# Kernel optimization log

Measured on AMD Instinct MI355X. Metric: run time of the kernel, lower is better.

## Reference

```python
import jax, jax.numpy as jnp
import numpy as np

B, S, D = 1, 2048, 2048
H, KVH, HD = 16, 4, 128  # n_heads, n_kv_heads, head_dim; n_rep = H // KVH
NEG = -1e9


def setup_inputs() -> dict:
    key = jax.random.key(0)
    ks = jax.random.split(key, 5)
    x = jax.random.normal(ks[0], (B, S, D), dtype=jnp.float32)
    sd = 1.0 / np.sqrt(D)
    wq = jax.random.normal(ks[1], (D, H * HD), dtype=jnp.float32) * sd
    wk = jax.random.normal(ks[2], (D, KVH * HD), dtype=jnp.float32) * sd
    wv = jax.random.normal(ks[3], (D, KVH * HD), dtype=jnp.float32) * sd
    wo = jax.random.normal(ks[4], (H * HD, D), dtype=jnp.float32) * sd
    # RoPE frequencies: theta = 10000, pairs of dims
    inv_freq = 1.0 / (10000.0 ** (jnp.arange(0, HD, 2, dtype=jnp.float32) / HD))  # [HD/2]
    t = jnp.arange(S, dtype=jnp.float32)
    freqs = jnp.outer(t, inv_freq)  # [S, HD/2]
    freqs_cos = jnp.cos(freqs)
    freqs_sin = jnp.sin(freqs)
    # additive causal mask [S, S]
    mask = jnp.where(jnp.tril(jnp.ones((S, S), dtype=bool)), 0.0, NEG).astype(jnp.float32)
    return {"x": x, "wq": wq, "wk": wk, "wv": wv, "wo": wo,
            "freqs_cos": freqs_cos, "freqs_sin": freqs_sin, "mask": mask}


def _rope(t, cos, sin):
    # t: [B, S, h, HD]; cos/sin: [S, HD/2] -> broadcast [1, S, 1, HD/2]
    tr = t.reshape(*t.shape[:-1], HD // 2, 2)
    t0, t1 = tr[..., 0], tr[..., 1]
    c = cos[None, :, None, :]
    s = sin[None, :, None, :]
    o0 = t0 * c - t1 * s
    o1 = t0 * s + t1 * c
    return jnp.stack([o0, o1], axis=-1).reshape(t.shape)


def reference(x, wq, wk, wv, wo, freqs_cos, freqs_sin, mask):
    n_rep = H // KVH
    xq = (x @ wq).reshape(B, S, H, HD)
    xk = (x @ wk).reshape(B, S, KVH, HD)
    xv = (x @ wv).reshape(B, S, KVH, HD)
    xq = _rope(xq, freqs_cos, freqs_sin)
    xk = _rope(xk, freqs_cos, freqs_sin)
    # repeat KV heads for GQA -> [B, S, H, HD]
    xk = jnp.repeat(xk, n_rep, axis=2)
    xv = jnp.repeat(xv, n_rep, axis=2)
    # [B, H, S, HD]
    q = xq.transpose(0, 2, 1, 3)
    k = xk.transpose(0, 2, 1, 3)
    v = xv.transpose(0, 2, 1, 3)
    scores = jnp.einsum('bhqd,bhkd->bhqk', q, k) / jnp.sqrt(jnp.float32(HD))
    scores = scores + mask[None, None, :, :]
    probs = jax.nn.softmax(scores.astype(jnp.float32), axis=-1).astype(q.dtype)
    out = jnp.einsum('bhqk,bhkd->bhqd', probs, v)
    out = out.transpose(0, 2, 1, 3).reshape(B, S, H * HD)
    return out @ wo
```

## Files before the change

### kernel.cpp

```cpp
#include <hip/hip_runtime.h>
#include <stdint.h>

#define S_LEN 2048
#define DMODEL 2048
#define NH 16
#define NKV 4
#define HD 128

typedef __attribute__((ext_vector_type(8))) short bf16x8_t;
typedef __attribute__((ext_vector_type(4))) short bf16x4_t;
typedef __attribute__((ext_vector_type(4))) float f32x4;

static __device__ __forceinline__ short f2bf(float f) {
  uint32_t x = __float_as_uint(f);
  uint32_t r = (x + 0x7FFFu + ((x >> 16) & 1u)) >> 16;
  return (short)r;
}

static __device__ __forceinline__ void gload16(const void* g, void* l) {
  __builtin_amdgcn_global_load_lds((const __attribute__((address_space(1))) void*)g,
                                   (__attribute__((address_space(3))) void*)l, 16, 0, 0);
}

__global__ void cvt_bf16(const float* __restrict__ in, short* __restrict__ out, int n8) {
  int idx = blockIdx.x * 256 + threadIdx.x;
  if (idx >= n8) return;
  const float4* p = (const float4*)in + 2 * (size_t)idx;
  float4 a = p[0], b = p[1];
  bf16x8_t o;
  o[0] = f2bf(a.x); o[1] = f2bf(a.y); o[2] = f2bf(a.z); o[3] = f2bf(a.w);
  o[4] = f2bf(b.x); o[5] = f2bf(b.y); o[6] = f2bf(b.z); o[7] = f2bf(b.w);
  ((bf16x8_t*)out)[idx] = o;
}

__global__ void transpose_f32_bf16(const float* __restrict__ in, short* __restrict__ out,
                                   int inStride, int outStride,
                                   long zInOff, long zOutOff) {
  __shared__ float tile[32][33];
  in  += (size_t)blockIdx.z * zInOff;
  out += (size_t)blockIdx.z * zOutOff;
  int c0 = blockIdx.x * 32, r0 = blockIdx.y * 32;
  int tx = threadIdx.x, ty = threadIdx.y;
  for (int i = ty; i < 32; i += 8)
    tile[i][tx] = in[(size_t)(r0 + i) * inStride + c0 + tx];
  __syncthreads();
  for (int i = ty; i < 32; i += 8)
    out[(size_t)(c0 + i) * outStride + r0 + tx] = f2bf(tile[tx][i]);
}

__global__ void rope_heads(const float* __restrict__ xf, const float* __restrict__ fc,
                           const float* __restrict__ fs, short* __restrict__ outp,
                           int rowStride) {
  int s = blockIdx.x;
  int i = threadIdx.x;
  int h = blockIdx.y * blockDim.y + threadIdx.y;
  float c = fc[s * 64 + i], sn = fs[s * 64 + i];
  const float* xr = xf + (size_t)s * rowStride + h * HD;
  float t0 = xr[2 * i], t1 = xr[2 * i + 1];
  float o0 = t0 * c - t1 * sn;
  float o1 = t0 * sn + t1 * c;
  short* orow = outp + ((size_t)h * S_LEN + s) * HD;
  uint32_t pk = (uint32_t)(uint16_t)f2bf(o0) | ((uint32_t)(uint16_t)f2bf(o1) << 16);
  *(uint32_t*)&orow[2 * i] = pk;
}

__global__ __launch_bounds__(128) void gemm_bt(const short* __restrict__ A,
                                               const short* __restrict__ Bt,
                                               float* __restrict__ C,
                                               int M, int N, int K) {
  __shared__ char smem[12288];
  const int tid = threadIdx.x;
  const int wid = tid >> 6, lane = tid & 63;
  const int lq = lane & 15, g = lane >> 4;
  const int bm = blockIdx.y * 128, bn = blockIdx.x * 64;

  f32x4 acc[4][4] = {};

  const short* Asrc[4];
  const short* Bsrc[2];
#pragma unroll
  for (int u = 0; u < 4; u++) {
    int p = wid * 64 + u * 128 + lane;
    Asrc[u] = A + (size_t)(bm + (p >> 2)) * K + (p & 3) * 8;
  }
#pragma unroll
  for (int u = 0; u < 2; u++) {
    int p = wid * 64 + u * 128 + lane;
    Bsrc[u] = Bt + (size_t)(bn + (p >> 2)) * K + (p & 3) * 8;
  }
  char* la = smem;
  char* lb = smem + 8192;

  for (int k0 = 0; k0 < K; k0 += 32) {
    __syncthreads();
#pragma unroll
    for (int u = 0; u < 4; u++)
      gload16(Asrc[u] + k0, la + wid * 1024 + u * 2048);
#pragma unroll
    for (int u = 0; u < 2; u++)
      gload16(Bsrc[u] + k0, lb + wid * 1024 + u * 2048);
    __syncthreads();
    bf16x8_t af[4], bfr[4];
#pragma unroll
    for (int mi = 0; mi < 4; mi++)
      af[mi] = *(const bf16x8_t*)(la + (wid * 64 + mi * 16 + lq) * 64 + g * 16);
#pragma unroll
    for (int ni = 0; ni < 4; ni++)
      bfr[ni] = *(const bf16x8_t*)(lb + (ni * 16 + lq) * 64 + g * 16);
#pragma unroll
    for (int mi = 0; mi < 4; mi++)
#pragma unroll
      for (int ni = 0; ni < 4; ni++)
        acc[mi][ni] = __builtin_amdgcn_mfma_f32_16x16x32_bf16(af[mi], bfr[ni], acc[mi][ni], 0, 0, 0);
  }
#pragma unroll
  for (int mi = 0; mi < 4; mi++) {
#pragma unroll
    for (int r = 0; r < 4; r++) {
      int row = bm + wid * 64 + mi * 16 + g * 4 + r;
      float* Crow = C + (size_t)row * N + bn;
#pragma unroll
      for (int ni = 0; ni < 4; ni++)
        Crow[ni * 16 + lq] = acc[mi][ni][r];
    }
  }
}

__global__ __launch_bounds__(128) void flash_attn(const short* __restrict__ Q,
                                                  const short* __restrict__ Kb,
                                                  const short* __restrict__ Vt,
                                                  short* __restrict__ Oatt) {
  __shared__ char smem[65536];
  const int h = blockIdx.y, kvh = h >> 2;
  const int pair = blockIdx.x;
  const int wid = threadIdx.x >> 6, lane = threadIdx.x & 63;
  const int lq = lane & 15, g = lane >> 4;
  const float scale2 = 0.0883883476483184f * 1.4426950408889634f;
  const short* Kh = Kb + (size_t)kvh * S_LEN * HD;
  const short* Vh = Vt + (size_t)kvh * HD * S_LEN;

  int kOff[8], vOff[8];
#pragma unroll
  for (int u = 0; u < 8; u++) {
    int p = wid * 64 + u * 128 + lane;
    int kr = p >> 4, kc = (p & 15) ^ (kr & 7);
    kOff[u] = kr * HD + kc * 8;
    int vd = p >> 3, vc = (p & 7) ^ (vd & 7);
    vOff[u] = vd * S_LEN + vc * 8;
  }
  const int swz = lq & 7;

  for (int pass = 0; pass < 2; pass++) {
    const int qi = pass ? (63 - pair) : pair;
    const int q0 = qi * 32 + wid * 16;
    const int ntiles = (qi >> 1) + 1;
    const int q_abs = q0 + lq;

    const short* Qb = Q + ((size_t)h * S_LEN + q0) * HD;
    bf16x8_t qf[4];
#pragma unroll
    for (int kk = 0; kk < 4; kk++)
      qf[kk] = *(const bf16x8_t*)(Qb + lq * HD + kk * 32 + g * 8);

    f32x4 oa[8] = {};
    float m_run = -1e30f, l_run = 0.f;

#pragma unroll
    for (int u = 0; u < 8; u++) {
      gload16(Kh + kOff[u], smem + wid * 1024 + u * 2048);
      gload16(Vh + vOff[u], smem + 16384 + wid * 1024 + u * 2048);
    }
    __syncthreads();

    for (int t = 0; t < ntiles; t++) {
      const int cur = t & 1;
      const int kv0 = t * 64;
      if (t + 1 < ntiles) {
        const short* Ks = Kh + (size_t)(kv0 + 64) * HD;
        const short* Vs = Vh + kv0 + 64;
        char* dk = smem + (cur ^ 1) * 32768;
        char* dv = dk + 16384;
#pragma unroll
        for (int u = 0; u < 8; u++) {
          gload16(Ks + kOff[u], dk + wid * 1024 + u * 2048);
          gload16(Vs + vOff[u], dv + wid * 1024 + u * 2048);
        }
      }
      const char* lk = smem + cur * 32768;
      const char* lv = lk + 16384;

      f32x4 sc[4] = {};
#pragma unroll
      for (int sub = 0; sub < 4; sub++) {
        const char* krow = lk + (sub * 16 + lq) * 256;
#pragma unroll
        for (int kk = 0; kk < 4; kk++) {
          bf16x8_t kf = *(const bf16x8_t*)(krow + (((kk * 4 + g) ^ swz) << 4));
          sc[sub] = __builtin_amdgcn_mfma_f32_16x16x32_bf16(kf, qf[kk], sc[sub], 0, 0, 0);
        }
      }
      float s16[16];
      if (t == ntiles - 1) {
#pragma unroll
        for (int sub = 0; sub < 4; sub++)
#pragma unroll
          for (int r = 0; r < 4; r++) {
            int kva = kv0 + sub * 16 + 4 * g + r;
            s16[sub * 4 + r] = (kva <= q_abs) ? sc[sub][r] * scale2 : -1e30f;
          }
      } else {
#pragma unroll
        for (int sub = 0; sub < 4; sub++)
#pragma unroll
          for (int r = 0; r < 4; r++)
            s16[sub * 4 + r] = sc[sub][r] * scale2;
      }
      float mx = s16[0];
#pragma unroll
      for (int j = 1; j < 16; j++) mx = fmaxf(mx, s16[j]);
      mx = fmaxf(mx, __shfl_xor(mx, 16));
      mx = fmaxf(mx, __shfl_xor(mx, 32));
      float m_new = fmaxf(m_run, mx);
      float p16[16], psum = 0.f;
#pragma unroll
      for (int j = 0; j < 16; j++) { p16[j] = exp2f(s16[j] - m_new); psum += p16[j]; }
      psum += __shfl_xor(psum, 16);
      psum += __shfl_xor(psum, 32);
      float f = exp2f(m_run - m_new);
      l_run = l_run * f + psum;
      m_run = m_new;

      bf16x8_t pf0, pf1;
#pragma unroll
      for (int j = 0; j < 8; j++) { pf0[j] = f2bf(p16[j]); pf1[j] = f2bf(p16[8 + j]); }
      float fr[4];
#pragma unroll
      for (int r = 0; r < 4; r++) fr[r] = __shfl(f, 4 * g + r);
#pragma unroll
      for (int nt = 0; nt < 8; nt++)
#pragma unroll
        for (int r = 0; r < 4; r++) oa[nt][r] *= fr[r];

      const int gh = g >> 1;
#pragma unroll
      for (int nt = 0; nt < 8; nt++) {
        const char* vrow = lv + (nt * 16 + lq) * 128 + (g & 1) * 8;
#pragma unroll
        for (int ks = 0; ks < 2; ks++) {
          bf16x4_t v0 = *(const bf16x4_t*)(vrow + (((ks * 4 + gh) ^ swz) << 4));
          bf16x4_t v1 = *(const bf16x4_t*)(vrow + (((ks * 4 + 2 + gh) ^ swz) << 4));
          bf16x8_t vf;
#pragma unroll
          for (int j = 0; j < 4; j++) { vf[j] = v0[j]; vf[4 + j] = v1[j]; }
          oa[nt] = __builtin_amdgcn_mfma_f32_16x16x32_bf16(ks ? pf1 : pf0, vf, oa[nt], 0, 0, 0);
        }
      }
      __syncthreads();
    }

    float lr[4];
#pragma unroll
    for (int r = 0; r < 4; r++) lr[r] = 1.0f / __shfl(l_run, 4 * g + r);
#pragma unroll
    for (int nt = 0; nt < 8; nt++)
#pragma unroll
      for (int r = 0; r < 4; r++) {
        int row = q0 + 4 * g + r;
        Oatt[(size_t)row * (NH * HD) + h * HD + nt * 16 + lq] = f2bf(oa[nt][r] * lr[r]);
      }
  }
}

extern "C" void kernel_launch(void* const* d_in, const int* in_sizes, int n_in,
                              void* d_out, int out_size, void* d_ws, size_t ws_size,
                              hipStream_t stream) {
  const float* x  = (const float*)d_in[0];
  const float* wq = (const float*)d_in[1];
  const float* wk = (const float*)d_in[2];
  const float* wv = (const float*)d_in[3];
  const float* wo = (const float*)d_in[4];
  const float* fc = (const float*)d_in[5];
  const float* fs = (const float*)d_in[6];
  float* out = (float*)d_out;

  char* ws = (char*)d_ws;
  const size_t MB = 1024 * 1024;
  if (ws_size < 72 * MB) return;
  short* xb    = (short*)(ws);
  short* wqkvT = (short*)(ws + 8 * MB);
  short* woT   = (short*)(ws + 20 * MB);
  float* xqkvf = (float*)(ws + 28 * MB);
  short* qbf   = (short*)(ws + 52 * MB);
  short* kbf   = (short*)(ws + 60 * MB);
  short* vT    = (short*)(ws + 62 * MB);
  short* abf   = (short*)(ws + 64 * MB);

  dim3 tb(32, 8);
  cvt_bf16<<<2048, 256, 0, stream>>>(x, xb, (S_LEN * DMODEL) / 8);
  transpose_f32_bf16<<<dim3(64, 64, 1), tb, 0, stream>>>(wq, wqkvT, 2048, 2048, 0, 0);
  transpose_f32_bf16<<<dim3(16, 64, 1), tb, 0, stream>>>(wk, wqkvT + (size_t)2048 * 2048, 512, 2048, 0, 0);
  transpose_f32_bf16<<<dim3(16, 64, 1), tb, 0, stream>>>(wv, wqkvT + (size_t)2560 * 2048, 512, 2048, 0, 0);
  transpose_f32_bf16<<<dim3(64, 64, 1), tb, 0, stream>>>(wo, woT, 2048, 2048, 0, 0);

  gemm_bt<<<dim3(48, 16), 128, 0, stream>>>(xb, wqkvT, xqkvf, 2048, 3072, 2048);

  rope_heads<<<dim3(2048, 4), dim3(64, 4), 0, stream>>>(xqkvf, fc, fs, qbf, 3072);
  rope_heads<<<dim3(2048, 1), dim3(64, 4), 0, stream>>>(xqkvf + 2048, fc, fs, kbf, 3072);
  transpose_f32_bf16<<<dim3(4, 64, 4), tb, 0, stream>>>(xqkvf + 2560, vT, 3072, 2048, 128, 128L * 2048);

  flash_attn<<<dim3(32, 16), 128, 0, stream>>>(qbf, kbf, vT, abf);

  gemm_bt<<<dim3(32, 16), 128, 0, stream>>>(abf, woT, out, 2048, 2048, 2048);
}
```

Baseline: 330.5 us.

## Emit bf16 QKV from GEMM, fold softmax scale into Q, restructure flash attention

The QKV GEMM now writes bf16 instead of fp32, so the rope and V-transpose kernels read half the bytes. The softmax scale is folded into Q during rope. Flash attention moves from 128-thread blocks that each process two paired 32-row query tiles with double-buffered K/V to 256-thread blocks handling one 64-row tile with a single buffer and 32KB of shared memory. It also adds a lazy rescale that skips the output correction when the running max rises by less than a threshold, plus s_setprio around the MFMA sections. The trade-off is an extra bf16 rounding of the QKV projections, loss of load/compute overlap, and causal imbalance because the pairing is dropped.

```diff
diff --git a/kernel.cpp b/kernel.cpp
--- a/kernel.cpp
+++ b/kernel.cpp
@@ -48,25 +48,43 @@
     out[(size_t)(c0 + i) * outStride + r0 + tx] = f2bf(tile[tx][i]);
 }
 
-__global__ void rope_heads(const float* __restrict__ xf, const float* __restrict__ fc,
+__global__ void transpose_bf16(const short* __restrict__ in, short* __restrict__ out,
+                               int inStride, int outStride,
+                               long zInOff, long zOutOff) {
+  __shared__ short tile[32][33];
+  in  += (size_t)blockIdx.z * zInOff;
+  out += (size_t)blockIdx.z * zOutOff;
+  int c0 = blockIdx.x * 32, r0 = blockIdx.y * 32;
+  int tx = threadIdx.x, ty = threadIdx.y;
+  for (int i = ty; i < 32; i += 8)
+    tile[i][tx] = in[(size_t)(r0 + i) * inStride + c0 + tx];
+  __syncthreads();
+  for (int i = ty; i < 32; i += 8)
+    out[(size_t)(c0 + i) * outStride + r0 + tx] = tile[tx][i];
+}
+
+__global__ void rope_heads(const short* __restrict__ xf, const float* __restrict__ fc,
                            const float* __restrict__ fs, short* __restrict__ outp,
-                           int rowStride) {
+                           int rowStride, float oscale) {
   int s = blockIdx.x;
   int i = threadIdx.x;
   int h = blockIdx.y * blockDim.y + threadIdx.y;
   float c = fc[s * 64 + i], sn = fs[s * 64 + i];
-  const float* xr = xf + (size_t)s * rowStride + h * HD;
-  float t0 = xr[2 * i], t1 = xr[2 * i + 1];
-  float o0 = t0 * c - t1 * sn;
-  float o1 = t0 * sn + t1 * c;
+  const short* xr = xf + (size_t)s * rowStride + h * HD;
+  uint32_t w = *(const uint32_t*)&xr[2 * i];
+  float t0 = __uint_as_float((w & 0xFFFFu) << 16);
+  float t1 = __uint_as_float(w & 0xFFFF0000u);
+  float o0 = (t0 * c - t1 * sn) * oscale;
+  float o1 = (t0 * sn + t1 * c) * oscale;
   short* orow = outp + ((size_t)h * S_LEN + s) * HD;
   uint32_t pk = (uint32_t)(uint16_t)f2bf(o0) | ((uint32_t)(uint16_t)f2bf(o1) << 16);
   *(uint32_t*)&orow[2 * i] = pk;
 }
 
+template <bool BF16OUT>
 __global__ __launch_bounds__(128) void gemm_bt(const short* __restrict__ A,
                                                const short* __restrict__ Bt,
-                                               float* __restrict__ C,
+                                               void* __restrict__ Cv,
                                                int M, int N, int K) {
   __shared__ char smem[12288];
   const int tid = threadIdx.x;
@@ -118,31 +136,38 @@
 #pragma unroll
     for (int r = 0; r < 4; r++) {
       int row = bm + wid * 64 + mi * 16 + g * 4 + r;
-      float* Crow = C + (size_t)row * N + bn;
-#pragma unroll
-      for (int ni = 0; ni < 4; ni++)
-        Crow[ni * 16 + lq] = acc[mi][ni][r];
-    }
-  }
-}
-
-__global__ __launch_bounds__(128) void flash_attn(const short* __restrict__ Q,
-                                                  const short* __restrict__ Kb,
-                                                  const short* __restrict__ Vt,
-                                                  short* __restrict__ Oatt) {
-  __shared__ char smem[65536];
+      if (BF16OUT) {
+        short* Crow = (short*)Cv + (size_t)row * N + bn;
+#pragma unroll
+        for (int ni = 0; ni < 4; ni++)
+          Crow[ni * 16 + lq] = f2bf(acc[mi][ni][r]);
+      } else {
+        float* Crow = (float*)Cv + (size_t)row * N + bn;
+#pragma unroll
+        for (int ni = 0; ni < 4; ni++)
+          Crow[ni * 16 + lq] = acc[mi][ni][r];
+      }
+    }
+  }
+}
+
+__global__ __launch_bounds__(256, 3) void flash_attn(const short* __restrict__ Q,
+                                                     const short* __restrict__ Kb,
+                                                     const short* __restrict__ Vt,
+                                                     short* __restrict__ Oatt) {
+  __shared__ char smem[32768];
   const int h = blockIdx.y, kvh = h >> 2;
-  const int pair = blockIdx.x;
-  const int wid = threadIdx.x >> 6, lane = threadIdx.x & 63;
+  const int qi = 31 - blockIdx.x;
+  const int tid = threadIdx.x;
+  const int wid = tid >> 6, lane = tid & 63;
   const int lq = lane & 15, g = lane >> 4;
-  const float scale2 = 0.0883883476483184f * 1.4426950408889634f;
   const short* Kh = Kb + (size_t)kvh * S_LEN * HD;
   const short* Vh = Vt + (size_t)kvh * HD * S_LEN;
 
-  int kOff[8], vOff[8];
-#pragma unroll
-  for (int u = 0; u < 8; u++) {
-    int p = wid * 64 + u * 128 + lane;
+  int kOff[4], vOff[4];
+#pragma unroll
+  for (int u = 0; u < 4; u++) {
+    int p = u * 256 + tid;
     int kr = p >> 4, kc = (p & 15) ^ (kr & 7);
     kOff[u] = kr * HD + kc * 8;
     int vd = p >> 3, vc = (p & 7) ^ (vd & 7);
@@ -150,125 +175,118 @@
   }
   const int swz = lq & 7;
 
-  for (int pass = 0; pass < 2; pass++) {
-    const int qi = pass ? (63 - pair) : pair;
-    const int q0 = qi * 32 + wid * 16;
-    const int ntiles = (qi >> 1) + 1;
-    const int q_abs = q0 + lq;
-
-    const short* Qb = Q + ((size_t)h * S_LEN + q0) * HD;
-    bf16x8_t qf[4];
-#pragma unroll
-    for (int kk = 0; kk < 4; kk++)
-      qf[kk] = *(const bf16x8_t*)(Qb + lq * HD + kk * 32 + g * 8);
-
-    f32x4 oa[8] = {};
-    float m_run = -1e30f, l_run = 0.f;
-
-#pragma unroll
-    for (int u = 0; u < 8; u++) {
-      gload16(Kh + kOff[u], smem + wid * 1024 + u * 2048);
-      gload16(Vh + vOff[u], smem + 16384 + wid * 1024 + u * 2048);
+  const int q0 = qi * 64 + wid * 16;
+  const int nt_ = qi + 1;
+  const int q_abs = q0 + lq;
+
+  const short* Qb = Q + ((size_t)h * S_LEN + q0) * HD;
+  bf16x8_t qf[4];
+#pragma unroll
+  for (int kk = 0; kk < 4; kk++)
+    qf[kk] = *(const bf16x8_t*)(Qb + lq * HD + kk * 32 + g * 8);
+
+  f32x4 oa[8] = {};
+  float m_run = -1e30f, l_run = 0.f;
+
+  for (int t = 0; t < nt_; ++t) {
+    const int kv0 = t * 64;
+    const short* Ks = Kh + (size_t)kv0 * HD;
+    const short* Vs = Vh + kv0;
+#pragma unroll
+    for (int u = 0; u < 4; u++) {
+      gload16(Ks + kOff[u], smem + u * 4096 + wid * 1024);
+      gload16(Vs + vOff[u], smem + 16384 + u * 4096 + wid * 1024);
     }
     __syncthreads();
 
-    for (int t = 0; t < ntiles; t++) {
-      const int cur = t & 1;
-      const int kv0 = t * 64;
-      if (t + 1 < ntiles) {
-        const short* Ks = Kh + (size_t)(kv0 + 64) * HD;
-        const short* Vs = Vh + kv0 + 64;
-        char* dk = smem + (cur ^ 1) * 32768;
-        char* dv = dk + 16384;
-#pragma unroll
-        for (int u = 0; u < 8; u++) {
-          gload16(Ks + kOff[u], dk + wid * 1024 + u * 2048);
-          gload16(Vs + vOff[u], dv + wid * 1024 + u * 2048);
+    f32x4 sc[4] = {};
+    __builtin_amdgcn_s_setprio(1);
+#pragma unroll
+    for (int sub = 0; sub < 4; sub++) {
+      const char* krow = smem + (sub * 16 + lq) * 256;
+#pragma unroll
+      for (int kk = 0; kk < 4; kk++) {
+        bf16x8_t kf = *(const bf16x8_t*)(krow + (((kk * 4 + g) ^ swz) << 4));
+        sc[sub] = __builtin_amdgcn_mfma_f32_16x16x32_bf16(kf, qf[kk], sc[sub], 0, 0, 0);
+      }
+    }
+    __builtin_amdgcn_s_setprio(0);
+
+    float s16[16];
+    if (t == nt_ - 1) {
+#pragma unroll
+      for (int sub = 0; sub < 4; sub++)
+#pragma unroll
+        for (int r = 0; r < 4; r++) {
+          int kva = kv0 + sub * 16 + 4 * g + r;
+          s16[sub * 4 + r] = (kva <= q_abs) ? sc[sub][r] : -1e30f;
         }
+    } else {
+#pragma unroll
+      for (int sub = 0; sub < 4; sub++)
+#pragma unroll
+        for (int r = 0; r < 4; r++)
+          s16[sub * 4 + r] = sc[sub][r];
+    }
+    float mx = s16[0];
+#pragma unroll
+    for (int j = 1; j < 16; j++) mx = fmaxf(mx, s16[j]);
+    mx = fmaxf(mx, __shfl_xor(mx, 16));
+    mx = fmaxf(mx, __shfl_xor(mx, 32));
+
+    if (!__all(mx <= m_run + 11.0f)) {
+      float m_new = fmaxf(m_run, mx);
+      float fl = exp2f(m_run - m_new);
+      float fr[4];
+#pragma unroll
+      for (int r = 0; r < 4; r++) fr[r] = __shfl(fl, 4 * g + r);
+#pragma unroll
+      for (int nt = 0; nt < 8; nt++)
+#pragma unroll
+        for (int r = 0; r < 4; r++) oa[nt][r] *= fr[r];
+      l_run *= fl;
+      m_run = m_new;
+    }
+    float p16[16], psum = 0.f;
+#pragma unroll
+    for (int j = 0; j < 16; j++) { p16[j] = exp2f(s16[j] - m_run); psum += p16[j]; }
+    psum += __shfl_xor(psum, 16);
+    psum += __shfl_xor(psum, 32);
+    l_run += psum;
+
+    bf16x8_t pf0, pf1;
+#pragma unroll
+    for (int j = 0; j < 8; j++) { pf0[j] = f2bf(p16[j]); pf1[j] = f2bf(p16[8 + j]); }
+
+    const int gh = g >> 1;
+    __builtin_amdgcn_s_setprio(1);
+#pragma unroll
+    for (int nt = 0; nt < 8; nt++) {
+      const char* vrow = smem + 16384 + (nt * 16 + lq) * 128 + (g & 1) * 8;
+#pragma unroll
+      for (int ks = 0; ks < 2; ks++) {
+        bf16x4_t v0 = *(const bf16x4_t*)(vrow + (((ks * 4 + gh) ^ swz) << 4));
+        bf16x4_t v1 = *(const bf16x4_t*)(vrow + (((ks * 4 + 2 + gh) ^ swz) << 4));
+        bf16x8_t vf;
+#pragma unroll
+        for (int j = 0; j < 4; j++) { vf[j] = v0[j]; vf[4 + j] = v1[j]; }
+        oa[nt] = __builtin_amdgcn_mfma_f32_16x16x32_bf16(ks ? pf1 : pf0, vf, oa[nt], 0, 0, 0);
       }
-      const char* lk = smem + cur * 32768;
-      const char* lv = lk + 16384;
-
-      f32x4 sc[4] = {};
-#pragma unroll
-      for (int sub = 0; sub < 4; sub++) {
-        const char* krow = lk + (sub * 16 + lq) * 256;
-#pragma unroll
-        for (int kk = 0; kk < 4; kk++) {
-          bf16x8_t kf = *(const bf16x8_t*)(krow + (((kk * 4 + g) ^ swz) << 4));
-          sc[sub] = __builtin_amdgcn_mfma_f32_16x16x32_bf16(kf, qf[kk], sc[sub], 0, 0, 0);
-        }
-      }
-      float s16[16];
-      if (t == ntiles - 1) {
-#pragma unroll
-        for (int sub = 0; sub < 4; sub++)
-#pragma unroll
-          for (int r = 0; r < 4; r++) {
-            int kva = kv0 + sub * 16 + 4 * g + r;
-            s16[sub * 4 + r] = (kva <= q_abs) ? sc[sub][r] * scale2 : -1e30f;
-          }
-      } else {
-#pragma unroll
-        for (int sub = 0; sub < 4; sub++)
-#pragma unroll
-          for (int r = 0; r < 4; r++)
-            s16[sub * 4 + r] = sc[sub][r] * scale2;
-      }
-      float mx = s16[0];
-#pragma unroll
-      for (int j = 1; j < 16; j++) mx = fmaxf(mx, s16[j]);
-      mx = fmaxf(mx, __shfl_xor(mx, 16));
-      mx = fmaxf(mx, __shfl_xor(mx, 32));
-      float m_new = fmaxf(m_run, mx);
-      float p16[16], psum = 0.f;
-#pragma unroll
-      for (int j = 0; j < 16; j++) { p16[j] = exp2f(s16[j] - m_new); psum += p16[j]; }
-      psum += __shfl_xor(psum, 16);
-      psum += __shfl_xor(psum, 32);
-      float f = exp2f(m_run - m_new);
-      l_run = l_run * f + psum;
-      m_run = m_new;
-
-      bf16x8_t pf0, pf1;
-#pragma unroll
-      for (int j = 0; j < 8; j++) { pf0[j] = f2bf(p16[j]); pf1[j] = f2bf(p16[8 + j]); }
-      float fr[4];
-#pragma unroll
-      for (int r = 0; r < 4; r++) fr[r] = __shfl(f, 4 * g + r);
-#pragma unroll
-      for (int nt = 0; nt < 8; nt++)
-#pragma unroll
-        for (int r = 0; r < 4; r++) oa[nt][r] *= fr[r];
-
-      const int gh = g >> 1;
-#pragma unroll
-      for (int nt = 0; nt < 8; nt++) {
-        const char* vrow = lv + (nt * 16 + lq) * 128 + (g & 1) * 8;
-#pragma unroll
-        for (int ks = 0; ks < 2; ks++) {
-          bf16x4_t v0 = *(const bf16x4_t*)(vrow + (((ks * 4 + gh) ^ swz) << 4));
-          bf16x4_t v1 = *(const bf16x4_t*)(vrow + (((ks * 4 + 2 + gh) ^ swz) << 4));
-          bf16x8_t vf;
-#pragma unroll
-          for (int j = 0; j < 4; j++) { vf[j] = v0[j]; vf[4 + j] = v1[j]; }
-          oa[nt] = __builtin_amdgcn_mfma_f32_16x16x32_bf16(ks ? pf1 : pf0, vf, oa[nt], 0, 0, 0);
-        }
-      }
-      __syncthreads();
-    }
-
-    float lr[4];
-#pragma unroll
-    for (int r = 0; r < 4; r++) lr[r] = 1.0f / __shfl(l_run, 4 * g + r);
-#pragma unroll
-    for (int nt = 0; nt < 8; nt++)
-#pragma unroll
-      for (int r = 0; r < 4; r++) {
-        int row = q0 + 4 * g + r;
-        Oatt[(size_t)row * (NH * HD) + h * HD + nt * 16 + lq] = f2bf(oa[nt][r] * lr[r]);
-      }
-  }
+    }
+    __builtin_amdgcn_s_setprio(0);
+    if (t + 1 < nt_) __syncthreads();
+  }
+
+  float lr[4];
+#pragma unroll
+  for (int r = 0; r < 4; r++) lr[r] = 1.0f / __shfl(l_run, 4 * g + r);
+#pragma unroll
+  for (int nt = 0; nt < 8; nt++)
+#pragma unroll
+    for (int r = 0; r < 4; r++) {
+      int row = q0 + 4 * g + r;
+      Oatt[(size_t)row * (NH * HD) + h * HD + nt * 16 + lq] = f2bf(oa[nt][r] * lr[r]);
+    }
 }
 
 extern "C" void kernel_launch(void* const* d_in, const int* in_sizes, int n_in,
@@ -285,15 +303,17 @@
 
   char* ws = (char*)d_ws;
   const size_t MB = 1024 * 1024;
-  if (ws_size < 72 * MB) return;
+  if (ws_size < 64 * MB) return;
   short* xb    = (short*)(ws);
   short* wqkvT = (short*)(ws + 8 * MB);
   short* woT   = (short*)(ws + 20 * MB);
-  float* xqkvf = (float*)(ws + 28 * MB);
-  short* qbf   = (short*)(ws + 52 * MB);
-  short* kbf   = (short*)(ws + 60 * MB);
-  short* vT    = (short*)(ws + 62 * MB);
-  short* abf   = (short*)(ws + 64 * MB);
+  short* xqkvb = (short*)(ws + 28 * MB);
+  short* qbf   = (short*)(ws + 40 * MB);
+  short* kbf   = (short*)(ws + 48 * MB);
+  short* vT    = (short*)(ws + 50 * MB);
+  short* abf   = (short*)(ws + 52 * MB);
+
+  const float scale2 = 0.0883883476483184f * 1.4426950408889634f;
 
   dim3 tb(32, 8);
   cvt_bf16<<<2048, 256, 0, stream>>>(x, xb, (S_LEN * DMODEL) / 8);
@@ -302,13 +322,13 @@
   transpose_f32_bf16<<<dim3(16, 64, 1), tb, 0, stream>>>(wv, wqkvT + (size_t)2560 * 2048, 512, 2048, 0, 0);
   transpose_f32_bf16<<<dim3(64, 64, 1), tb, 0, stream>>>(wo, woT, 2048, 2048, 0, 0);
 
-  gemm_bt<<<dim3(48, 16), 128, 0, stream>>>(xb, wqkvT, xqkvf, 2048, 3072, 2048);
-
-  rope_heads<<<dim3(2048, 4), dim3(64, 4), 0, stream>>>(xqkvf, fc, fs, qbf, 3072);
-  rope_heads<<<dim3(2048, 1), dim3(64, 4), 0, stream>>>(xqkvf + 2048, fc, fs, kbf, 3072);
-  transpose_f32_bf16<<<dim3(4, 64, 4), tb, 0, stream>>>(xqkvf + 2560, vT, 3072, 2048, 128, 128L * 2048);
-
-  flash_attn<<<dim3(32, 16), 128, 0, stream>>>(qbf, kbf, vT, abf);
-
-  gemm_bt<<<dim3(32, 16), 128, 0, stream>>>(abf, woT, out, 2048, 2048, 2048);
-}
+  gemm_bt<true><<<dim3(48, 16), 128, 0, stream>>>(xb, wqkvT, xqkvb, 2048, 3072, 2048);
+
+  rope_heads<<<dim3(2048, 4), dim3(64, 4), 0, stream>>>(xqkvb, fc, fs, qbf, 3072, scale2);
+  rope_heads<<<dim3(2048, 1), dim3(64, 4), 0, stream>>>(xqkvb + 2048, fc, fs, kbf, 3072, 1.0f);
+  transpose_bf16<<<dim3(4, 64, 4), tb, 0, stream>>>(xqkvb + 2560, vT, 3072, 2048, 128, 128L * 2048);
+
+  flash_attn<<<dim3(32, 16), 256, 0, stream>>>(qbf, kbf, vT, abf);
+
+  gemm_bt<false><<<dim3(32, 16), 128, 0, stream>>>(abf, woT, out, 2048, 2048, 2048);
+}
```

Measured after the change: 323.4 us. 2.1% less time.
